# Performance work log

Hardware: AMD Instinct MI355X
Metric: run time of the kernel (lower is better)

## Reference

```python
import jax, jax.numpy as jnp
import numpy as np

HEADS = 2
OUT_CH = 128
NEG_SLOPE_ATT = 0.2   # GATv2Conv attention LeakyReLU
NEG_SLOPE_ACT = 0.01  # nn.LeakyReLU default
BN_EPS = 1e-5


def setup_inputs() -> dict:
    key = jax.random.key(0)
    ks = jax.random.split(key, 8)
    B, C, D, H, W = 2, 128, 8, 32, 32
    N = B * D * H * W            # 16384 graph nodes
    E = 196608                   # avg degree 12
    x = jax.random.normal(ks[0], (B, C, D, H, W), dtype=jnp.float32)
    edge_index = jax.random.randint(ks[1], (2, E), 0, N, dtype=jnp.int64)
    lin_w = jax.random.normal(ks[2], (C, HEADS * OUT_CH), dtype=jnp.float32) * (1.0 / np.sqrt(C))
    lin_b = jax.random.normal(ks[3], (HEADS * OUT_CH,), dtype=jnp.float32) * 0.02
    att = jax.random.normal(ks[4], (HEADS, OUT_CH), dtype=jnp.float32) * (1.0 / np.sqrt(OUT_CH))
    gat_bias = jax.random.normal(ks[5], (OUT_CH,), dtype=jnp.float32) * 0.02
    bn_gamma = jnp.ones((OUT_CH,), dtype=jnp.float32)
    bn_beta = jnp.zeros((OUT_CH,), dtype=jnp.float32)
    return {"x": x, "edge_index": edge_index, "lin_w": lin_w, "lin_b": lin_b,
            "att": att, "gat_bias": gat_bias, "bn_gamma": bn_gamma, "bn_beta": bn_beta}


def _gatv2(xf, src, dst, lin_w, lin_b, att, gat_bias, n_nodes):
    # shared-weights GATv2: x' = x W + b, per edge e=(j->i): score = a . lrelu(x'_i + x'_j)
    h = (xf @ lin_w + lin_b).reshape(n_nodes, HEADS, OUT_CH)  # [N, H, C]
    x_src = h[src]                                            # [E, H, C] messages
    logits = jnp.einsum('ehc,hc->eh', jax.nn.leaky_relu(x_src + h[dst], NEG_SLOPE_ATT), att)
    # segment softmax over edges sharing the same target node
    m = jax.ops.segment_max(logits, dst, num_segments=n_nodes)      # [N, H]
    ex = jnp.exp(logits - m[dst])
    denom = jax.ops.segment_sum(ex, dst, num_segments=n_nodes)      # [N, H]
    alpha = ex / denom[dst]
    out = jax.ops.segment_sum(x_src * alpha[..., None], dst, num_segments=n_nodes)  # [N, H, C]
    return out.mean(axis=1) + gat_bias  # concat=False -> head mean


def reference(x, edge_index, lin_w, lin_b, att, gat_bias, bn_gamma, bn_beta):
    B, C, D, H, W = x.shape
    N = B * D * H * W
    xf = x.reshape(B, C, -1).transpose(0, 2, 1).reshape(N, C)
    # add_self_loops=True (PyG default)
    loop = jnp.arange(N, dtype=edge_index.dtype)
    src = jnp.concatenate([edge_index[0], loop])
    dst = jnp.concatenate([edge_index[1], loop])
    out = _gatv2(xf, src, dst, lin_w, lin_b, att, gat_bias, N)      # [N, OUT_CH]
    out = out.reshape(B, D * H * W, OUT_CH).transpose(0, 2, 1).reshape(B, OUT_CH, D, H, W)
    # BatchNorm3d (training-mode batch stats, biased variance)
    mean = out.mean(axis=(0, 2, 3, 4), keepdims=True)
    var = out.var(axis=(0, 2, 3, 4), keepdims=True)
    out = (out - mean) / jnp.sqrt(var + BN_EPS)
    out = out * bn_gamma.reshape(1, -1, 1, 1, 1) + bn_beta.reshape(1, -1, 1, 1, 1)
    return jax.nn.leaky_relu(out, NEG_SLOPE_ACT)
```

## Files before the change

### kernel.cpp

```cpp
#include <hip/hip_runtime.h>
#include <math.h>

#define N_NODES 16384
#define CIN 128
#define HOUT 256
#define OUTC 128
#define NEG_ATT 0.2f
#define NEG_ACT 0.01f
#define BN_EPS 1e-5f
#define ELLW 64
#define GEMM_BLOCKS 1024

typedef short short8 __attribute__((ext_vector_type(8)));
typedef float f32x4 __attribute__((ext_vector_type(4)));

static __device__ __forceinline__ unsigned short f2bf(float f) {
    unsigned int u = __float_as_uint(f);
    unsigned int r = (u + 0x7FFFu + ((u >> 16) & 1u)) >> 16;
    return (unsigned short)r;
}
static __device__ __forceinline__ void unpack8(uint4 u, float* f) {
    f[0] = __uint_as_float(u.x << 16);
    f[1] = __uint_as_float(u.x & 0xffff0000u);
    f[2] = __uint_as_float(u.y << 16);
    f[3] = __uint_as_float(u.y & 0xffff0000u);
    f[4] = __uint_as_float(u.z << 16);
    f[5] = __uint_as_float(u.z & 0xffff0000u);
    f[6] = __uint_as_float(u.w << 16);
    f[7] = __uint_as_float(u.w & 0xffff0000u);
}
template <int CTRL>
static __device__ __forceinline__ float dppadd(float x) {
    return x + __int_as_float(__builtin_amdgcn_update_dpp(
        0, __float_as_int(x), CTRL, 0xF, 0xF, true));
}
#define DPP_XOR1 0xB1
#define DPP_XOR2 0x4E
#define DPP_HMIR 0x141
#define DPP_MIR  0x140

#define LDP 136
__global__ __launch_bounds__(256) void gemm_scatter_kernel(const float* __restrict__ x,
                                                           const float* __restrict__ lin_w,
                                                           const float* __restrict__ lin_b,
                                                           unsigned short* __restrict__ h,
                                                           const int* __restrict__ edges,
                                                           int* __restrict__ deg,
                                                           int* __restrict__ ell,
                                                           float* __restrict__ gz, int E) {
    __shared__ __align__(16) unsigned short A_s[64 * LDP];
    __shared__ __align__(16) unsigned short Bt_s[64 * LDP];
    const int t = threadIdx.x;
    const int bid = blockIdx.x;

    if (bid >= GEMM_BLOCKS) {
        int e = (bid - GEMM_BLOCKS) * 256 + t;
        if (e < E) {
            int s = edges[e];
            int d = edges[E + e];
            int slot = atomicAdd(&deg[d], 1);
            if (slot < ELLW) ell[(d << 6) + slot] = s;
        }
        return;
    }

    if (bid == 0) gz[t] = 0.f;

    const int node0 = (bid >> 2) * 64;
    const int o0 = (bid & 3) * 64;
    const int b = node0 >> 13;
    const int s0 = node0 & 8191;

    const int nt = t & 15;
    const int kt = t >> 4;
#pragma unroll
    for (int p = 0; p < 2; p++) {
        const int kb = p * 64 + kt * 4;
        float4 ar[4], br[4];
#pragma unroll
        for (int r = 0; r < 4; r++) {
            ar[r] = *(const float4*)&x[((b * CIN + kb + r) << 13) + s0 + nt * 4];
            br[r] = *(const float4*)&lin_w[(kb + r) * HOUT + o0 + nt * 4];
        }
#pragma unroll
        for (int j = 0; j < 4; j++) {
            ushort4 va, vb;
            va.x = f2bf(((const float*)&ar[0])[j]);
            va.y = f2bf(((const float*)&ar[1])[j]);
            va.z = f2bf(((const float*)&ar[2])[j]);
            va.w = f2bf(((const float*)&ar[3])[j]);
            vb.x = f2bf(((const float*)&br[0])[j]);
            vb.y = f2bf(((const float*)&br[1])[j]);
            vb.z = f2bf(((const float*)&br[2])[j]);
            vb.w = f2bf(((const float*)&br[3])[j]);
            *(ushort4*)&A_s[(nt * 4 + j) * LDP + kb] = va;
            *(ushort4*)&Bt_s[(nt * 4 + j) * LDP + kb] = vb;
        }
    }
    __syncthreads();

    const int w = t >> 6;
    const int lane = t & 63;
    const int lrow = lane & 15;
    const int lquad = lane >> 4;
    const int m0 = w * 16;

    short8 afr[4];
#pragma unroll
    for (int ks = 0; ks < 4; ks++)
        afr[ks] = *(const short8*)&A_s[(m0 + lrow) * LDP + ks * 32 + lquad * 8];

    f32x4 acc[4];
#pragma unroll
    for (int c = 0; c < 4; c++) { acc[c][0] = 0.f; acc[c][1] = 0.f; acc[c][2] = 0.f; acc[c][3] = 0.f; }

#pragma unroll
    for (int c = 0; c < 4; c++) {
#pragma unroll
        for (int ks = 0; ks < 4; ks++) {
            short8 bfr = *(const short8*)&Bt_s[(c * 16 + lrow) * LDP + ks * 32 + lquad * 8];
            acc[c] = __builtin_amdgcn_mfma_f32_16x16x32_bf16(afr[ks], bfr, acc[c], 0, 0, 0);
        }
    }

#pragma unroll
    for (int c = 0; c < 4; c++) {
        const int col = o0 + c * 16 + lrow;
        const float lb = lin_b[col];
#pragma unroll
        for (int r = 0; r < 4; r++) {
            const int n = node0 + m0 + lquad * 4 + r;
            h[n * HOUT + col] = f2bf(acc[c][r] + lb);
        }
    }
}

__global__ __launch_bounds__(256) void gat_kernel(const unsigned short* __restrict__ h,
                                                  const int* __restrict__ deg,
                                                  const int* __restrict__ ell,
                                                  const float* __restrict__ att,
                                                  const float* __restrict__ gat_bias,
                                                  float* __restrict__ gat,
                                                  float* __restrict__ gsum,
                                                  float* __restrict__ gsumsq) {
    const int t = threadIdx.x;
    const int lane = t & 63;
    const int w = t >> 6;
    const int half = lane >> 5;
    const int sub = lane & 31;
    const int c0 = sub * 8;

    __shared__ float ssum[128], ssq[128];
    if (t < 128) { ssum[t] = 0.f; ssq[t] = 0.f; }
    __syncthreads();

    const int nodes0 = (blockIdx.x << 4) + (w << 2);
    uint4 hdr[4];
#pragma unroll
    for (int i = 0; i < 4; i++)
        hdr[i] = *(const uint4*)&h[(nodes0 + i) * HOUT + c0];
    int4 dg4 = *(const int4*)&deg[nodes0];
    int dgs[4] = {dg4.x, dg4.y, dg4.z, dg4.w};

    float av[8];
    *(float4*)&av[0] = *(const float4*)&att[c0];
    *(float4*)&av[4] = *(const float4*)&att[c0 + 4];
#pragma unroll
    for (int c = 0; c < 8; c++) av[c] *= 1.44269504f;
    float gb[8];
    *(float4*)&gb[0] = *(const float4*)&gat_bias[c0 & 127];
    *(float4*)&gb[4] = *(const float4*)&gat_bias[(c0 & 127) + 4];

    float st[8] = {}, sq[8] = {};

    for (int i = 0; i < 4; i++) {
        const int node = nodes0 + i;
        float hd[8];
        unpack8(hdr[i], hd);
        const int cnt = (dgs[i] < ELLW ? dgs[i] : ELLW);
        const int* __restrict__ row = &ell[node << 6];

        float ds = 0.f;
#pragma unroll
        for (int c = 0; c < 8; c++) {
            float v = 2.f * hd[c];
            v = fmaxf(v, NEG_ATT * v);
            ds = fmaf(v, av[c], ds);
        }
        ds = dppadd<DPP_XOR1>(ds);
        ds = dppadd<DPP_XOR2>(ds);
        ds = dppadd<DPP_HMIR>(ds);
        ds = dppadd<DPP_MIR>(ds);
        float wself = (half == 0) ? exp2f(ds) : 0.f;
        float denom = wself;
        float acc[8];
#pragma unroll
        for (int c = 0; c < 8; c++) acc[c] = wself * hd[c];

        int jn[4];
#pragma unroll
        for (int u = 0; u < 4; u++) {
            int e = 2 * u + half;
            jn[u] = (e < cnt) ? row[e] : node;
        }

        for (int base = 0; base < cnt; base += 8) {
            int jc[4];
#pragma unroll
            for (int u = 0; u < 4; u++) jc[u] = jn[u];
#pragma unroll
            for (int u = 0; u < 4; u++) {
                int e = base + 8 + 2 * u + half;
                jn[u] = (e < cnt) ? row[e] : node;
            }
            float hj[4][8];
#pragma unroll
            for (int u = 0; u < 4; u++)
                unpack8(*(const uint4*)&h[jc[u] * HOUT + c0], hj[u]);
            float p[4];
#pragma unroll
            for (int u = 0; u < 4; u++) {
                float d = 0.f;
#pragma unroll
                for (int c = 0; c < 8; c++) {
                    float v = hj[u][c] + hd[c];
                    v = fmaxf(v, NEG_ATT * v);
                    d = fmaf(v, av[c], d);
                }
                p[u] = d;
            }
#pragma unroll
            for (int u = 0; u < 4; u++) p[u] = dppadd<DPP_XOR1>(p[u]);
#pragma unroll
            for (int u = 0; u < 4; u++) p[u] = dppadd<DPP_XOR2>(p[u]);
#pragma unroll
            for (int u = 0; u < 4; u++) p[u] = dppadd<DPP_HMIR>(p[u]);
#pragma unroll
            for (int u = 0; u < 4; u++) p[u] = dppadd<DPP_MIR>(p[u]);
#pragma unroll
            for (int u = 0; u < 4; u++) {
                float wt = ((base + 2 * u + half) < cnt) ? exp2f(p[u]) : 0.f;
                denom += wt;
#pragma unroll
                for (int c = 0; c < 8; c++) acc[c] = fmaf(wt, hj[u][c], acc[c]);
            }
        }
        denom += __shfl_xor(denom, 32);
#pragma unroll
        for (int c = 0; c < 8; c++) acc[c] += __shfl_xor(acc[c], 32);
        float inv = 1.0f / denom;
        float r[8];
#pragma unroll
        for (int c = 0; c < 8; c++) r[c] = acc[c] * inv;
#pragma unroll
        for (int c = 0; c < 8; c++) r[c] += __shfl_xor(r[c], 16);
        if (lane < 16) {
            float o[8];
#pragma unroll
            for (int c = 0; c < 8; c++) {
                o[c] = 0.5f * r[c] + gb[c];
                st[c] += o[c];
                sq[c] += o[c] * o[c];
            }
            *(float4*)&gat[node * OUTC + c0] = *(float4*)&o[0];
            *(float4*)&gat[node * OUTC + c0 + 4] = *(float4*)&o[4];
        }
    }
    if (lane < 16) {
#pragma unroll
        for (int c = 0; c < 8; c++) {
            atomicAdd(&ssum[c0 + c], st[c]);
            atomicAdd(&ssq[c0 + c], sq[c]);
        }
    }
    __syncthreads();
    if (t < 128) {
        atomicAdd(&gsum[t], ssum[t]);
        atomicAdd(&gsumsq[t], ssq[t]);
    }
}

__global__ __launch_bounds__(256) void epilogue_kernel(const float* __restrict__ gat,
                                                       const float* __restrict__ gsum,
                                                       const float* __restrict__ gsumsq,
                                                       const float* __restrict__ gamma,
                                                       const float* __restrict__ beta,
                                                       float* __restrict__ out) {
    __shared__ float tile[64 * 129];
    __shared__ float sc[128], sh[128];
    const int t = threadIdx.x;
    if (t < 128) {
        const float invN = 1.0f / (float)N_NODES;
        float mean = gsum[t] * invN;
        float var = gsumsq[t] * invN - mean * mean;
        float rstd = rsqrtf(var + BN_EPS);
        float s = gamma[t] * rstd;
        sc[t] = s;
        sh[t] = beta[t] - mean * s;
    }
    __syncthreads();
    const int n0 = blockIdx.x * 64;
    const int b = n0 >> 13;
    const int s0 = n0 & 8191;
#pragma unroll
    for (int k = 0; k < 32; k++) {
        int f = t + k * 256;
        int nl = f >> 7;
        int c = f & 127;
        float v = gat[(n0 << 7) + f];
        v = v * sc[c] + sh[c];
        v = v > 0.f ? v : NEG_ACT * v;
        tile[nl * 129 + c] = v;
    }
    __syncthreads();
    const int sl = t & 63;
    const int c0 = t >> 6;
#pragma unroll
    for (int k = 0; k < 32; k++) {
        int c = c0 + (k << 2);
        out[((b * OUTC + c) << 13) + s0 + sl] = tile[sl * 129 + c];
    }
}

extern "C" void kernel_launch(void* const* d_in, const int* in_sizes, int n_in,
                              void* d_out, int out_size, void* d_ws, size_t ws_size,
                              hipStream_t stream) {
    const float* x        = (const float*)d_in[0];
    const int*   edges    = (const int*)d_in[1];
    const float* lin_w    = (const float*)d_in[2];
    const float* lin_b    = (const float*)d_in[3];
    const float* att      = (const float*)d_in[4];
    const float* gat_bias = (const float*)d_in[5];
    const float* bn_gamma = (const float*)d_in[6];
    const float* bn_beta  = (const float*)d_in[7];
    float* out = (float*)d_out;
    int E = in_sizes[1] / 2;

    char* ws = (char*)d_ws;
    unsigned short* h = (unsigned short*)(ws);
    float* gat     = (float*)(ws + 8388608);
    int*   deg     = (int*)(ws + 16777216);
    int*   ell     = (int*)(ws + 16842752);
    float* gsum    = (float*)(ws + 21037056);
    float* gsumsq  = gsum + 128;

    hipMemsetAsync(deg, 0, N_NODES * sizeof(int), stream);
    const int scatter_blocks = (E + 255) / 256;
    gemm_scatter_kernel<<<GEMM_BLOCKS + scatter_blocks, 256, 0, stream>>>(
        x, lin_w, lin_b, h, edges, deg, ell, gsum, E);
    gat_kernel<<<N_NODES / 16, 256, 0, stream>>>(h, deg, ell, att, gat_bias, gat, gsum, gsumsq);
    epilogue_kernel<<<N_NODES / 64, 256, 0, stream>>>(gat, gsum, gsumsq, bn_gamma, bn_beta, out);
}
```

Measured before the change: 135.3 us.

## Split each node's edge list across two wavefronts and merge partials in LDS

Each group of four nodes is now handled by two wavefronts. Each wavefront processes an interleaved half of the neighbor list, and their partial accumulators and denominators are combined through shared memory after a block barrier. The grid doubles to N/8 blocks. The aim is to halve the serial gather-loop length per wave and add more parallelism to hide gather latency. The cost is extra LDS traffic (about 16KB per block), an added barrier, and a finalization phase in which half the waves sit idle.

```diff
diff --git a/kernel.cpp b/kernel.cpp
--- a/kernel.cpp
+++ b/kernel.cpp
@@ -146,15 +146,18 @@
     const int t = threadIdx.x;
     const int lane = t & 63;
     const int w = t >> 6;
+    const int ns = w >> 1;
+    const int part = w & 1;
     const int half = lane >> 5;
     const int sub = lane & 31;
     const int c0 = sub * 8;
 
+    __shared__ float pacc[2][2][4][256];
+    __shared__ float pden[2][2][4][2];
     __shared__ float ssum[128], ssq[128];
     if (t < 128) { ssum[t] = 0.f; ssq[t] = 0.f; }
-    __syncthreads();
-
-    const int nodes0 = (blockIdx.x << 4) + (w << 2);
+
+    const int nodes0 = (blockIdx.x << 3) + (ns << 2);
     uint4 hdr[4];
 #pragma unroll
     for (int i = 0; i < 4; i++)
@@ -167,11 +170,6 @@
     *(float4*)&av[4] = *(const float4*)&att[c0 + 4];
 #pragma unroll
     for (int c = 0; c < 8; c++) av[c] *= 1.44269504f;
-    float gb[8];
-    *(float4*)&gb[0] = *(const float4*)&gat_bias[c0 & 127];
-    *(float4*)&gb[4] = *(const float4*)&gat_bias[(c0 & 127) + 4];
-
-    float st[8] = {}, sq[8] = {};
 
     for (int i = 0; i < 4; i++) {
         const int node = nodes0 + i;
@@ -180,37 +178,41 @@
         const int cnt = (dgs[i] < ELLW ? dgs[i] : ELLW);
         const int* __restrict__ row = &ell[node << 6];
 
-        float ds = 0.f;
-#pragma unroll
-        for (int c = 0; c < 8; c++) {
-            float v = 2.f * hd[c];
-            v = fmaxf(v, NEG_ATT * v);
-            ds = fmaf(v, av[c], ds);
-        }
-        ds = dppadd<DPP_XOR1>(ds);
-        ds = dppadd<DPP_XOR2>(ds);
-        ds = dppadd<DPP_HMIR>(ds);
-        ds = dppadd<DPP_MIR>(ds);
-        float wself = (half == 0) ? exp2f(ds) : 0.f;
-        float denom = wself;
-        float acc[8];
-#pragma unroll
-        for (int c = 0; c < 8; c++) acc[c] = wself * hd[c];
-
+        float denom = 0.f;
+        float acc[8] = {};
+        if (part == 0) {
+            float ds = 0.f;
+#pragma unroll
+            for (int c = 0; c < 8; c++) {
+                float v = 2.f * hd[c];
+                v = fmaxf(v, NEG_ATT * v);
+                ds = fmaf(v, av[c], ds);
+            }
+            ds = dppadd<DPP_XOR1>(ds);
+            ds = dppadd<DPP_XOR2>(ds);
+            ds = dppadd<DPP_HMIR>(ds);
+            ds = dppadd<DPP_MIR>(ds);
+            float wself = (half == 0) ? exp2f(ds) : 0.f;
+            denom = wself;
+#pragma unroll
+            for (int c = 0; c < 8; c++) acc[c] = wself * hd[c];
+        }
+
+        const int soff = 2 * part + half;
         int jn[4];
 #pragma unroll
         for (int u = 0; u < 4; u++) {
-            int e = 2 * u + half;
+            int e = 4 * u + soff;
             jn[u] = (e < cnt) ? row[e] : node;
         }
 
-        for (int base = 0; base < cnt; base += 8) {
+        for (int base = 0; base < cnt; base += 16) {
             int jc[4];
 #pragma unroll
             for (int u = 0; u < 4; u++) jc[u] = jn[u];
 #pragma unroll
             for (int u = 0; u < 4; u++) {
-                int e = base + 8 + 2 * u + half;
+                int e = base + 16 + 4 * u + soff;
                 jn[u] = (e < cnt) ? row[e] : node;
             }
             float hj[4][8];
@@ -239,7 +241,7 @@
             for (int u = 0; u < 4; u++) p[u] = dppadd<DPP_MIR>(p[u]);
 #pragma unroll
             for (int u = 0; u < 4; u++) {
-                float wt = ((base + 2 * u + half) < cnt) ? exp2f(p[u]) : 0.f;
+                float wt = ((base + 4 * u + soff) < cnt) ? exp2f(p[u]) : 0.f;
                 denom += wt;
 #pragma unroll
                 for (int c = 0; c < 8; c++) acc[c] = fmaf(wt, hj[u][c], acc[c]);
@@ -248,29 +250,49 @@
         denom += __shfl_xor(denom, 32);
 #pragma unroll
         for (int c = 0; c < 8; c++) acc[c] += __shfl_xor(acc[c], 32);
-        float inv = 1.0f / denom;
-        float r[8];
-#pragma unroll
-        for (int c = 0; c < 8; c++) r[c] = acc[c] * inv;
-#pragma unroll
-        for (int c = 0; c < 8; c++) r[c] += __shfl_xor(r[c], 16);
+        if (lane < 32) {
+#pragma unroll
+            for (int c = 0; c < 8; c++) pacc[part][ns][i][c * 32 + sub] = acc[c];
+        }
+        if (lane < 32 && (lane & 15) == 0)
+            pden[part][ns][i][lane >> 4] = denom;
+    }
+    __syncthreads();
+
+    float st[8] = {}, sq[8] = {};
+    if (part == 0) {
+        float gb[8];
+        *(float4*)&gb[0] = *(const float4*)&gat_bias[c0 & 127];
+        *(float4*)&gb[4] = *(const float4*)&gat_bias[(c0 & 127) + 4];
+        const int hh = sub >> 4;
+        for (int i = 0; i < 4; i++) {
+            const int node = nodes0 + i;
+            float den = pden[0][ns][i][hh] + pden[1][ns][i][hh];
+            float inv = 1.0f / den;
+            float r[8];
+#pragma unroll
+            for (int c = 0; c < 8; c++)
+                r[c] = (pacc[0][ns][i][c * 32 + sub] + pacc[1][ns][i][c * 32 + sub]) * inv;
+#pragma unroll
+            for (int c = 0; c < 8; c++) r[c] += __shfl_xor(r[c], 16);
+            if (lane < 16) {
+                float o[8];
+#pragma unroll
+                for (int c = 0; c < 8; c++) {
+                    o[c] = 0.5f * r[c] + gb[c];
+                    st[c] += o[c];
+                    sq[c] += o[c] * o[c];
+                }
+                *(float4*)&gat[node * OUTC + c0] = *(float4*)&o[0];
+                *(float4*)&gat[node * OUTC + c0 + 4] = *(float4*)&o[4];
+            }
+        }
         if (lane < 16) {
-            float o[8];
 #pragma unroll
             for (int c = 0; c < 8; c++) {
-                o[c] = 0.5f * r[c] + gb[c];
-                st[c] += o[c];
-                sq[c] += o[c] * o[c];
-            }
-            *(float4*)&gat[node * OUTC + c0] = *(float4*)&o[0];
-            *(float4*)&gat[node * OUTC + c0 + 4] = *(float4*)&o[4];
-        }
-    }
-    if (lane < 16) {
-#pragma unroll
-        for (int c = 0; c < 8; c++) {
-            atomicAdd(&ssum[c0 + c], st[c]);
-            atomicAdd(&ssq[c0 + c], sq[c]);
+                atomicAdd(&ssum[c0 + c], st[c]);
+                atomicAdd(&ssq[c0 + c], sq[c]);
+            }
         }
     }
     __syncthreads();
@@ -348,6 +370,6 @@
     const int scatter_blocks = (E + 255) / 256;
     gemm_scatter_kernel<<<GEMM_BLOCKS + scatter_blocks, 256, 0, stream>>>(
         x, lin_w, lin_b, h, edges, deg, ell, gsum, E);
-    gat_kernel<<<N_NODES / 16, 256, 0, stream>>>(h, deg, ell, att, gat_bias, gat, gsum, gsumsq);
+    gat_kernel<<<N_NODES / 8, 256, 0, stream>>>(h, deg, ell, att, gat_bias, gat, gsum, gsumsq);
     epilogue_kernel<<<N_NODES / 64, 256, 0, stream>>>(gat, gsum, gsumsq, bn_gamma, bn_beta, out);
 }
```

After: 156.7 us. 1.16x slower.
